# Performance work log

Hardware: AMD Instinct MI355X
Metric: run time of the kernel (lower is better)

Reference implementation:

```python
import jax, jax.numpy as jnp
import numpy as np

NEG = -9e15
ALPHA = 0.2  # leaky_relu negative slope


def setup_inputs() -> dict:
    key = jax.random.key(0)
    k1, k2, k3, k4, k5 = jax.random.split(key, 5)
    N, F_in, F_out = 8192, 128, 128
    x = jax.random.normal(k1, (N, F_in), dtype=jnp.float32)
    adj = jax.random.randint(k2, (N, N), 0, 2).astype(jnp.float32)
    # xavier-ish scaled params
    W = jax.random.normal(k3, (F_in, F_out), dtype=jnp.float32) * (1.0 / np.sqrt(F_in))
    a1 = jax.random.normal(k4, (F_out,), dtype=jnp.float32) * (1.0 / np.sqrt(2 * F_out))
    a2 = jax.random.normal(k5, (F_out,), dtype=jnp.float32) * (1.0 / np.sqrt(2 * F_out))
    a_bias = jnp.zeros((1,), dtype=jnp.float32)
    return {"x": x, "adj": adj, "W": W, "a1": a1, "a2": a2, "a_bias": a_bias}


def reference(x, adj, W, a1, a2, a_bias):
    # h = W(input)                                   [N, F]
    h = x @ W
    # a(concat(h_i, h_j)) == h_i.a1 + h_j.a2 + b  -> avoids N*N*2F concat
    s1 = h @ a1  # [N]
    s2 = h @ a2  # [N]
    e = jax.nn.leaky_relu(s1[:, None] + s2[None, :] + a_bias[0], negative_slope=ALPHA)  # [N, N]
    e = jnp.where(adj > 0, e, NEG)
    attention = jax.nn.softmax(e, axis=1)
    # dropout p=0 (deterministic eval): identity
    return attention @ h
```

## Files before the change

kernel.cpp:

```cpp
#include <hip/hip_runtime.h>
#include <hip/hip_bf16.h>

typedef __attribute__((ext_vector_type(8)))  __bf16         bf16x8;
typedef __attribute__((ext_vector_type(4)))  float          f32x4;
typedef __attribute__((ext_vector_type(8)))  unsigned short u16x8;

#define LOG2E 1.44269504088896340736f

#if __has_builtin(__builtin_amdgcn_exp2f)
#define EXP2F(x) __builtin_amdgcn_exp2f(x)
#else
#define EXP2F(x) __builtin_exp2f(x)
#endif

__device__ __forceinline__ unsigned short f2b(float f) {
  union { __bf16 h; unsigned short s; } o; o.h = (__bf16)f; return o.s;
}

__global__ __launch_bounds__(256) void k_prep(
    const float* __restrict__ x, const float* __restrict__ W,
    const float* __restrict__ a1, const float* __restrict__ a2,
    const float* __restrict__ ab,
    unsigned short* __restrict__ hT, float* __restrict__ s1p,
    float* __restrict__ s2p) {
  __shared__ __align__(16) float Ws[64 * 128];
  __shared__ __align__(16) float Xs[16 * 128];
  const int t = threadIdx.x;
  const int rb = blockIdx.x * 16;
  const int r  = t >> 4;
  const int fg = t & 15;

  {
    int off = t * 8;
    *(f32x4*)(Xs + off)     = *(const f32x4*)(x + (long)rb * 128 + off);
    *(f32x4*)(Xs + off + 4) = *(const f32x4*)(x + (long)rb * 128 + off + 4);
  }

  float acc[8];
#pragma unroll
  for (int j = 0; j < 8; ++j) acc[j] = 0.f;

  for (int half = 0; half < 2; ++half) {
    __syncthreads();
#pragma unroll
    for (int c = 0; c < 8; ++c) {
      int off = c * 1024 + t * 4;
      *(f32x4*)(Ws + off) = *(const f32x4*)(W + half * 8192 + off);
    }
    __syncthreads();
    for (int k = 0; k < 64; ++k) {
      float xv = Xs[r * 128 + half * 64 + k];
      f32x4 w0 = *(const f32x4*)(Ws + k * 128 + fg * 8);
      f32x4 w1 = *(const f32x4*)(Ws + k * 128 + fg * 8 + 4);
#pragma unroll
      for (int j = 0; j < 4; ++j) {
        acc[j]     += xv * w0[j];
        acc[4 + j] += xv * w1[j];
      }
    }
  }

  float p1 = 0.f, p2 = 0.f;
#pragma unroll
  for (int j = 0; j < 8; ++j) {
    p1 += acc[j] * a1[fg * 8 + j];
    p2 += acc[j] * a2[fg * 8 + j];
  }
#pragma unroll
  for (int mask = 1; mask <= 8; mask <<= 1) {
    p1 += __shfl_xor(p1, mask, 64);
    p2 += __shfl_xor(p2, mask, 64);
  }
  if (fg == 0) {
    s1p[rb + r] = LOG2E * (p1 + ab[0]);
    s2p[rb + r] = LOG2E * p2;
  }
#pragma unroll
  for (int j = 0; j < 8; ++j)
    hT[(long)(fg * 8 + j) * 8192 + rb + r] = f2b(acc[j]);
}

__global__ __launch_bounds__(512, 2) void k_attn(
    const float* __restrict__ adj, const unsigned short* __restrict__ hT,
    const float* __restrict__ s1p, const float* __restrict__ s2p,
    float* __restrict__ out) {
  __shared__ __align__(16) unsigned short Bs[128 * 128];
  __shared__ __align__(16) unsigned short As[32 * 136];
  __shared__ float dens[32];

  const int t = threadIdx.x;
  const int i0 = blockIdx.x * 32;
  const int lane = t & 63;
  const int wv = t >> 6;
  const int r  = t >> 4;
  const int kc = t & 15;
  const int m    = lane & 15;
  const int quad = lane >> 4;
  const int rt = wv & 1;
  const int f0 = (wv >> 1) * 32;

  const float s1v = s1p[i0 + r];
  const float* adjp = adj + (long)(i0 + r) * 8192 + kc * 8;
  const float* s2pp = s2p + kc * 8;

  f32x4 acc0, acc1;
#pragma unroll
  for (int p = 0; p < 4; ++p) { acc0[p] = 0.f; acc1[p] = 0.f; }
  float den = 0.f;

  f32x4 ar0 = __builtin_nontemporal_load((const f32x4*)(adjp));
  f32x4 ar1 = __builtin_nontemporal_load((const f32x4*)(adjp + 4));
  f32x4 cs0 = *(const f32x4*)(s2pp);
  f32x4 cs1 = *(const f32x4*)(s2pp + 4);
  u16x8 stg[4];
#pragma unroll
  for (int rr = 0; rr < 4; ++rr) {
    int f = rr * 32 + r;
    int cg = kc ^ (f & 7);
    stg[rr] = *(const u16x8*)(hT + (long)f * 8192 + cg * 8);
  }

  for (int it = 0; it < 64; ++it) {
#pragma unroll
    for (int rr = 0; rr < 4; ++rr) {
      int f = rr * 32 + r;
      *(u16x8*)(Bs + f * 128 + kc * 8) = stg[rr];
    }
    const int itn = (it + 1) & 63;
    f32x4 nr0 = __builtin_nontemporal_load((const f32x4*)(adjp + (long)itn * 128));
    f32x4 nr1 = __builtin_nontemporal_load((const f32x4*)(adjp + (long)itn * 128 + 4));
    f32x4 ns0 = *(const f32x4*)(s2pp + itn * 128);
    f32x4 ns1 = *(const f32x4*)(s2pp + itn * 128 + 4);

    u16x8 w;
    float dloc = 0.f;
#pragma unroll
    for (int j = 0; j < 4; ++j) {
      float tp = s1v + cs0[j];
      float wval = ar0[j] * EXP2F(fmaxf(tp, 0.2f * tp));
      dloc += wval; w[j] = f2b(wval);
    }
#pragma unroll
    for (int j = 0; j < 4; ++j) {
      float tp = s1v + cs1[j];
      float wval = ar1[j] * EXP2F(fmaxf(tp, 0.2f * tp));
      dloc += wval; w[4 + j] = f2b(wval);
    }
    den += dloc;
    *(u16x8*)(As + r * 136 + kc * 8) = w;

    __syncthreads();

    if (it < 63) {
      const unsigned short* hTi = hT + (long)(it + 1) * 128;
#pragma unroll
      for (int rr = 0; rr < 4; ++rr) {
        int f = rr * 32 + r;
        int cg = kc ^ (f & 7);
        stg[rr] = *(const u16x8*)(hTi + (long)f * 8192 + cg * 8);
      }
    }

#pragma unroll
    for (int ks = 0; ks < 4; ++ks) {
      bf16x8 af = *(const bf16x8*)(As + (rt * 16 + m) * 136 + ks * 32 + quad * 8);
      int c = ks * 4 + quad;
      {
        int f = f0 + m;
        int slot = c ^ (f & 7);
        bf16x8 bv = *(const bf16x8*)(Bs + f * 128 + slot * 8);
        acc0 = __builtin_amdgcn_mfma_f32_16x16x32_bf16(af, bv, acc0, 0, 0, 0);
      }
      {
        int f = f0 + 16 + m;
        int slot = c ^ (f & 7);
        bf16x8 bv = *(const bf16x8*)(Bs + f * 128 + slot * 8);
        acc1 = __builtin_amdgcn_mfma_f32_16x16x32_bf16(af, bv, acc1, 0, 0, 0);
      }
    }
    __syncthreads();

    ar0 = nr0; ar1 = nr1; cs0 = ns0; cs1 = ns1;
  }

  den += __shfl_xor(den, 1, 64);
  den += __shfl_xor(den, 2, 64);
  den += __shfl_xor(den, 4, 64);
  den += __shfl_xor(den, 8, 64);
  if (kc == 0) dens[r] = den;
  __syncthreads();

#pragma unroll
  for (int p = 0; p < 4; ++p) {
    int row = rt * 16 + quad * 4 + p;
    float d = dens[row];
    float inv = (d != 0.f) ? (1.f / d) : 0.f;
    out[(long)(i0 + row) * 128 + f0 + m]      = acc0[p] * inv;
    out[(long)(i0 + row) * 128 + f0 + 16 + m] = acc1[p] * inv;
  }
}

extern "C" void kernel_launch(void* const* d_in, const int* in_sizes, int n_in,
                              void* d_out, int out_size, void* d_ws, size_t ws_size,
                              hipStream_t stream) {
  int ix = 0, iadj = 1, iw = 2, ia1 = 3, ia2 = 4, iab = 5;
  {
    int f128[2] = {-1, -1};
    int tx = -1, tadj = -1, tw = -1, tab = -1, n128 = 0;
    for (int i = 0; i < n_in; ++i) {
      int s = in_sizes[i];
      if (s == 67108864) tadj = i;
      else if (s == 1048576) tx = i;
      else if (s == 16384) tw = i;
      else if (s == 128 && n128 < 2) f128[n128++] = i;
      else if (s == 1) tab = i;
    }
    if (tx >= 0 && tadj >= 0 && tw >= 0 && tab >= 0 && n128 == 2) {
      ix = tx; iadj = tadj; iw = tw; ia1 = f128[0]; ia2 = f128[1]; iab = tab;
    }
  }
  const float* x   = (const float*)d_in[ix];
  const float* adj = (const float*)d_in[iadj];
  const float* W   = (const float*)d_in[iw];
  const float* a1  = (const float*)d_in[ia1];
  const float* a2  = (const float*)d_in[ia2];
  const float* ab  = (const float*)d_in[iab];

  char* ws = (char*)d_ws;
  unsigned short* hT = (unsigned short*)(ws);
  float* s1p = (float*)(ws + 2097152);
  float* s2p = (float*)(ws + 2097152 + 32768);

  k_prep<<<dim3(512), dim3(256), 0, stream>>>(x, W, a1, a2, ab, hT, s1p, s2p);
  k_attn<<<dim3(256), dim3(512), 0, stream>>>(adj, hT, s1p, s2p, (float*)d_out);
}
```

Measured before the change: 389.9 us.

## Double-buffer attention LDS tiles and halve rows per block to drop a barrier

The attention kernel now processes 16 rows per block with 256 threads and 512 blocks, so hT tile traffic is spread over twice as many blocks. A and B tiles in shared memory are double-buffered, which removes the second __syncthreads per iteration. Each thread now stages 8 hT vectors instead of 4. This doubles total hT reads from L2 per output row and raises LDS use per block, which may limit occupancy.

```diff
diff --git a/kernel.cpp b/kernel.cpp
--- a/kernel.cpp
+++ b/kernel.cpp
@@ -80,28 +80,29 @@
     hT[(long)(fg * 8 + j) * 8192 + rb + r] = f2b(acc[j]);
 }
 
-__global__ __launch_bounds__(512, 2) void k_attn(
+__global__ __launch_bounds__(256, 2) void k_attn(
     const float* __restrict__ adj, const unsigned short* __restrict__ hT,
     const float* __restrict__ s1p, const float* __restrict__ s2p,
     float* __restrict__ out) {
-  __shared__ __align__(16) unsigned short Bs[128 * 128];
-  __shared__ __align__(16) unsigned short As[32 * 136];
-  __shared__ float dens[32];
+  __shared__ __align__(16) unsigned short Bs[2][128 * 128];
+  __shared__ __align__(16) unsigned short As[2][16 * 136];
+  __shared__ float dens[16];
 
   const int t = threadIdx.x;
-  const int i0 = blockIdx.x * 32;
+  const int i0 = blockIdx.x * 16;
   const int lane = t & 63;
   const int wv = t >> 6;
   const int r  = t >> 4;
   const int kc = t & 15;
   const int m    = lane & 15;
   const int quad = lane >> 4;
-  const int rt = wv & 1;
-  const int f0 = (wv >> 1) * 32;
+  const int f0 = wv * 32;
+  const int cg = kc ^ (r & 7);
 
   const float s1v = s1p[i0 + r];
   const float* adjp = adj + (long)(i0 + r) * 8192 + kc * 8;
   const float* s2pp = s2p + kc * 8;
+  const unsigned short* hTb = hT + (long)r * 8192 + cg * 8;
 
   f32x4 acc0, acc1;
 #pragma unroll
@@ -112,25 +113,18 @@
   f32x4 ar1 = __builtin_nontemporal_load((const f32x4*)(adjp + 4));
   f32x4 cs0 = *(const f32x4*)(s2pp);
   f32x4 cs1 = *(const f32x4*)(s2pp + 4);
-  u16x8 stg[4];
-#pragma unroll
-  for (int rr = 0; rr < 4; ++rr) {
-    int f = rr * 32 + r;
-    int cg = kc ^ (f & 7);
-    stg[rr] = *(const u16x8*)(hT + (long)f * 8192 + cg * 8);
-  }
+  u16x8 stg[8];
+#pragma unroll
+  for (int rr = 0; rr < 8; ++rr)
+    stg[rr] = *(const u16x8*)(hTb + (long)rr * 131072);
 
   for (int it = 0; it < 64; ++it) {
-#pragma unroll
-    for (int rr = 0; rr < 4; ++rr) {
-      int f = rr * 32 + r;
-      *(u16x8*)(Bs + f * 128 + kc * 8) = stg[rr];
-    }
-    const int itn = (it + 1) & 63;
-    f32x4 nr0 = __builtin_nontemporal_load((const f32x4*)(adjp + (long)itn * 128));
-    f32x4 nr1 = __builtin_nontemporal_load((const f32x4*)(adjp + (long)itn * 128 + 4));
-    f32x4 ns0 = *(const f32x4*)(s2pp + itn * 128);
-    f32x4 ns1 = *(const f32x4*)(s2pp + itn * 128 + 4);
+    unsigned short* Bsb = &Bs[it & 1][0];
+    unsigned short* Asb = &As[it & 1][0];
+
+#pragma unroll
+    for (int rr = 0; rr < 8; ++rr)
+      *(u16x8*)(Bsb + (rr * 16 + r) * 128 + kc * 8) = stg[rr];
 
     u16x8 w;
     float dloc = 0.f;
@@ -147,40 +141,33 @@
       dloc += wval; w[4 + j] = f2b(wval);
     }
     den += dloc;
-    *(u16x8*)(As + r * 136 + kc * 8) = w;
+    *(u16x8*)(Asb + r * 136 + kc * 8) = w;
 
     __syncthreads();
 
-    if (it < 63) {
-      const unsigned short* hTi = hT + (long)(it + 1) * 128;
-#pragma unroll
-      for (int rr = 0; rr < 4; ++rr) {
-        int f = rr * 32 + r;
-        int cg = kc ^ (f & 7);
-        stg[rr] = *(const u16x8*)(hTi + (long)f * 8192 + cg * 8);
-      }
-    }
+    const int itn = (it + 1) & 63;
+    ar0 = __builtin_nontemporal_load((const f32x4*)(adjp + (long)itn * 128));
+    ar1 = __builtin_nontemporal_load((const f32x4*)(adjp + (long)itn * 128 + 4));
+    cs0 = *(const f32x4*)(s2pp + itn * 128);
+    cs1 = *(const f32x4*)(s2pp + itn * 128 + 4);
+    const unsigned short* hTi = hTb + itn * 128;
+#pragma unroll
+    for (int rr = 0; rr < 8; ++rr)
+      stg[rr] = *(const u16x8*)(hTi + (long)rr * 131072);
 
 #pragma unroll
     for (int ks = 0; ks < 4; ++ks) {
-      bf16x8 af = *(const bf16x8*)(As + (rt * 16 + m) * 136 + ks * 32 + quad * 8);
-      int c = ks * 4 + quad;
+      bf16x8 af = *(const bf16x8*)(Asb + m * 136 + ks * 32 + quad * 8);
+      int slot = (ks * 4 + quad) ^ (m & 7);
       {
-        int f = f0 + m;
-        int slot = c ^ (f & 7);
-        bf16x8 bv = *(const bf16x8*)(Bs + f * 128 + slot * 8);
+        bf16x8 bv = *(const bf16x8*)(Bsb + (f0 + m) * 128 + slot * 8);
         acc0 = __builtin_amdgcn_mfma_f32_16x16x32_bf16(af, bv, acc0, 0, 0, 0);
       }
       {
-        int f = f0 + 16 + m;
-        int slot = c ^ (f & 7);
-        bf16x8 bv = *(const bf16x8*)(Bs + f * 128 + slot * 8);
+        bf16x8 bv = *(const bf16x8*)(Bsb + (f0 + 16 + m) * 128 + slot * 8);
         acc1 = __builtin_amdgcn_mfma_f32_16x16x32_bf16(af, bv, acc1, 0, 0, 0);
       }
     }
-    __syncthreads();
-
-    ar0 = nr0; ar1 = nr1; cs0 = ns0; cs1 = ns1;
   }
 
   den += __shfl_xor(den, 1, 64);
@@ -192,7 +179,7 @@
 
 #pragma unroll
   for (int p = 0; p < 4; ++p) {
-    int row = rt * 16 + quad * 4 + p;
+    int row = quad * 4 + p;
     float d = dens[row];
     float inv = (d != 0.f) ? (1.f / d) : 0.f;
     out[(long)(i0 + row) * 128 + f0 + m]      = acc0[p] * inv;
@@ -232,5 +219,5 @@
   float* s2p = (float*)(ws + 2097152 + 32768);
 
   k_prep<<<dim3(512), dim3(256), 0, stream>>>(x, W, a1, a2, ab, hT, s1p, s2p);
-  k_attn<<<dim3(256), dim3(512), 0, stream>>>(adj, hT, s1p, s2p, (float*)d_out);
-}
+  k_attn<<<dim3(512), dim3(256), 0, stream>>>(adj, hT, s1p, s2p, (float*)d_out);
+}
```

After: 403.1 us. +3.4%, slower.

## Split attention neighbor dimension across two blocks and combine partials

Applied to the files above, without the earlier changes.

Each row-block of the attention kernel is split into two halves over the neighbor (column) dimension, doubling the grid to expose more parallelism for streaming the adjacency matrix. Partial numerators and denominators are written to workspace and a new combine kernel sums and normalizes them. Launch bounds are raised to allow more resident blocks per CU, which tightens the register budget and may cause spills; the extra pass adds traffic for the partial outputs.

```diff
diff --git a/kernel.cpp b/kernel.cpp
--- a/kernel.cpp
+++ b/kernel.cpp
@@ -80,16 +80,17 @@
     hT[(long)(fg * 8 + j) * 8192 + rb + r] = f2b(acc[j]);
 }
 
-__global__ __launch_bounds__(512, 2) void k_attn(
+__global__ __launch_bounds__(512, 4) void k_attn(
     const float* __restrict__ adj, const unsigned short* __restrict__ hT,
     const float* __restrict__ s1p, const float* __restrict__ s2p,
-    float* __restrict__ out) {
+    float* __restrict__ pout, float* __restrict__ pden) {
   __shared__ __align__(16) unsigned short Bs[128 * 128];
   __shared__ __align__(16) unsigned short As[32 * 136];
-  __shared__ float dens[32];
 
   const int t = threadIdx.x;
-  const int i0 = blockIdx.x * 32;
+  const int i0 = (blockIdx.x >> 1) * 32;
+  const int jh = blockIdx.x & 1;
+  const long jbase = (long)jh * 4096;
   const int lane = t & 63;
   const int wv = t >> 6;
   const int r  = t >> 4;
@@ -100,8 +101,8 @@
   const int f0 = (wv >> 1) * 32;
 
   const float s1v = s1p[i0 + r];
-  const float* adjp = adj + (long)(i0 + r) * 8192 + kc * 8;
-  const float* s2pp = s2p + kc * 8;
+  const float* adjp = adj + (long)(i0 + r) * 8192 + jbase + kc * 8;
+  const float* s2pp = s2p + jbase + kc * 8;
 
   f32x4 acc0, acc1;
 #pragma unroll
@@ -117,16 +118,16 @@
   for (int rr = 0; rr < 4; ++rr) {
     int f = rr * 32 + r;
     int cg = kc ^ (f & 7);
-    stg[rr] = *(const u16x8*)(hT + (long)f * 8192 + cg * 8);
-  }
-
-  for (int it = 0; it < 64; ++it) {
+    stg[rr] = *(const u16x8*)(hT + (long)f * 8192 + jbase + cg * 8);
+  }
+
+  for (int it = 0; it < 32; ++it) {
 #pragma unroll
     for (int rr = 0; rr < 4; ++rr) {
       int f = rr * 32 + r;
       *(u16x8*)(Bs + f * 128 + kc * 8) = stg[rr];
     }
-    const int itn = (it + 1) & 63;
+    const int itn = (it + 1) & 31;
     f32x4 nr0 = __builtin_nontemporal_load((const f32x4*)(adjp + (long)itn * 128));
     f32x4 nr1 = __builtin_nontemporal_load((const f32x4*)(adjp + (long)itn * 128 + 4));
     f32x4 ns0 = *(const f32x4*)(s2pp + itn * 128);
@@ -151,8 +152,8 @@
 
     __syncthreads();
 
-    if (it < 63) {
-      const unsigned short* hTi = hT + (long)(it + 1) * 128;
+    if (it < 31) {
+      const unsigned short* hTi = hT + jbase + (long)(it + 1) * 128;
 #pragma unroll
       for (int rr = 0; rr < 4; ++rr) {
         int f = rr * 32 + r;
@@ -187,17 +188,30 @@
   den += __shfl_xor(den, 2, 64);
   den += __shfl_xor(den, 4, 64);
   den += __shfl_xor(den, 8, 64);
-  if (kc == 0) dens[r] = den;
-  __syncthreads();
-
+  if (kc == 0) pden[jh * 8192 + i0 + r] = den;
+
+  float* po = pout + (long)jh * 1048576;
 #pragma unroll
   for (int p = 0; p < 4; ++p) {
     int row = rt * 16 + quad * 4 + p;
-    float d = dens[row];
-    float inv = (d != 0.f) ? (1.f / d) : 0.f;
-    out[(long)(i0 + row) * 128 + f0 + m]      = acc0[p] * inv;
-    out[(long)(i0 + row) * 128 + f0 + 16 + m] = acc1[p] * inv;
-  }
+    po[(long)(i0 + row) * 128 + f0 + m]      = acc0[p];
+    po[(long)(i0 + row) * 128 + f0 + 16 + m] = acc1[p];
+  }
+}
+
+__global__ __launch_bounds__(256) void k_comb(
+    const float* __restrict__ pout, const float* __restrict__ pden,
+    float* __restrict__ out) {
+  int g = blockIdx.x * 256 + threadIdx.x;
+  int i = g >> 5;
+  f32x4 a = *(const f32x4*)(pout + (long)g * 4);
+  f32x4 b = *(const f32x4*)(pout + 1048576 + (long)g * 4);
+  float d = pden[i] + pden[8192 + i];
+  float inv = (d != 0.f) ? (1.f / d) : 0.f;
+  f32x4 o;
+#pragma unroll
+  for (int p = 0; p < 4; ++p) o[p] = (a[p] + b[p]) * inv;
+  *(f32x4*)(out + (long)g * 4) = o;
 }
 
 extern "C" void kernel_launch(void* const* d_in, const int* in_sizes, int n_in,
@@ -228,9 +242,12 @@
 
   char* ws = (char*)d_ws;
   unsigned short* hT = (unsigned short*)(ws);
-  float* s1p = (float*)(ws + 2097152);
-  float* s2p = (float*)(ws + 2097152 + 32768);
+  float* s1p  = (float*)(ws + 2097152);
+  float* s2p  = (float*)(ws + 2097152 + 32768);
+  float* pout = (float*)(ws + 2162688);
+  float* pden = (float*)(ws + 2162688 + 8388608);
 
   k_prep<<<dim3(512), dim3(256), 0, stream>>>(x, W, a1, a2, ab, hT, s1p, s2p);
-  k_attn<<<dim3(256), dim3(512), 0, stream>>>(adj, hT, s1p, s2p, (float*)d_out);
-}
+  k_attn<<<dim3(512), dim3(512), 0, stream>>>(adj, hT, s1p, s2p, pout, pden);
+  k_comb<<<dim3(1024), dim3(256), 0, stream>>>(pout, pden, (float*)d_out);
+}
```

After: 390.7 us. No clear change (+0.2%).
